# Kernel tuning notes

Hardware: AMD Instinct MI355X
Metric: run time of the kernel (lower is better)

The kernel has to match this reference:

```python
import jax, jax.numpy as jnp
import numpy as np
import math

N_EMBD = 1024
N_HEAD = 16
B, T, T_PLAN = 2, 2048, 512
EPS = 1e-5


def _layernorm(x, g, b):
    m = jnp.mean(x, axis=-1, keepdims=True)
    v = jnp.mean(jnp.square(x - m), axis=-1, keepdims=True)
    return (x - m) * jax.lax.rsqrt(v + EPS) * g + b


def setup_inputs() -> dict:
    key = jax.random.key(0)
    ks = jax.random.split(key, 16)
    C = N_EMBD
    s = 0.02
    inp = {
        "x": jax.random.normal(ks[0], (B, T, C), jnp.float32),
        "plan_hidden": jax.random.normal(ks[1], (B, T_PLAN, C), jnp.float32),
        "ln1_g": jnp.ones((C,), jnp.float32), "ln1_b": jnp.zeros((C,), jnp.float32),
        # weights stored as [in, out] (torch Linear applies x @ W.T)
        "c_attn_w": s * jax.random.normal(ks[2], (C, 3 * C), jnp.float32),
        "c_attn_b": jnp.zeros((3 * C,), jnp.float32),
        "attn_proj_w": s * jax.random.normal(ks[3], (C, C), jnp.float32),
        "attn_proj_b": jnp.zeros((C,), jnp.float32),
        "ln2_g": jnp.ones((C,), jnp.float32), "ln2_b": jnp.zeros((C,), jnp.float32),
        "q_w": s * jax.random.normal(ks[4], (C, C), jnp.float32), "q_b": jnp.zeros((C,), jnp.float32),
        "k_w": s * jax.random.normal(ks[5], (C, C), jnp.float32), "k_b": jnp.zeros((C,), jnp.float32),
        "v_w": s * jax.random.normal(ks[6], (C, C), jnp.float32), "v_b": jnp.zeros((C,), jnp.float32),
        "ca_proj_w": s * jax.random.normal(ks[7], (C, C), jnp.float32),
        "ca_proj_b": jnp.zeros((C,), jnp.float32),
        "ln3_g": jnp.ones((C,), jnp.float32), "ln3_b": jnp.zeros((C,), jnp.float32),
        "fc_w": s * jax.random.normal(ks[8], (C, 4 * C), jnp.float32),
        "fc_b": jnp.zeros((4 * C,), jnp.float32),
        "mlp_proj_w": s * jax.random.normal(ks[9], (4 * C, C), jnp.float32),
        "mlp_proj_b": jnp.zeros((C,), jnp.float32),
    }
    return inp


def _split_heads(t, n_head):  # [B,T,C] -> [B,H,T,D]
    Bs, Ts, Cs = t.shape
    return t.reshape(Bs, Ts, n_head, Cs // n_head).transpose(0, 2, 1, 3)


def _merge_heads(t):  # [B,H,T,D] -> [B,T,C]
    Bs, H, Ts, D = t.shape
    return t.transpose(0, 2, 1, 3).reshape(Bs, Ts, H * D)


def _self_attn(x, c_attn_w, c_attn_b, proj_w, proj_b):
    Bs, Ts, C = x.shape
    qkv = x @ c_attn_w + c_attn_b
    q, k, v = jnp.split(qkv, 3, axis=-1)
    q, k, v = (_split_heads(t, N_HEAD) for t in (q, k, v))
    scale = 1.0 / math.sqrt(C // N_HEAD)
    att = jnp.einsum("bhqd,bhkd->bhqk", q, k) * scale
    mask = jnp.tril(jnp.ones((Ts, Ts), bool))
    att = jnp.where(mask, att, -jnp.inf)
    att = jax.nn.softmax(att, axis=-1)
    y = jnp.einsum("bhqk,bhkd->bhqd", att, v)
    return _merge_heads(y) @ proj_w + proj_b


def _cross_attn(x, plan, q_w, q_b, k_w, k_b, v_w, v_b, proj_w, proj_b):
    C = x.shape[-1]
    q = _split_heads(x @ q_w + q_b, N_HEAD)
    k = _split_heads(plan @ k_w + k_b, N_HEAD)
    v = _split_heads(plan @ v_w + v_b, N_HEAD)
    scale = 1.0 / math.sqrt(C // N_HEAD)
    att = jax.nn.softmax(jnp.einsum("bhqd,bhkd->bhqk", q, k) * scale, axis=-1)
    y = jnp.einsum("bhqk,bhkd->bhqd", att, v)
    return _merge_heads(y) @ proj_w + proj_b


def reference(x, plan_hidden, ln1_g, ln1_b, c_attn_w, c_attn_b, attn_proj_w, attn_proj_b,
              ln2_g, ln2_b, q_w, q_b, k_w, k_b, v_w, v_b, ca_proj_w, ca_proj_b,
              ln3_g, ln3_b, fc_w, fc_b, mlp_proj_w, mlp_proj_b):
    x = x + _self_attn(_layernorm(x, ln1_g, ln1_b), c_attn_w, c_attn_b, attn_proj_w, attn_proj_b)
    x = x + _cross_attn(_layernorm(x, ln2_g, ln2_b), plan_hidden,
                        q_w, q_b, k_w, k_b, v_w, v_b, ca_proj_w, ca_proj_b)
    h = _layernorm(x, ln3_g, ln3_b)
    h = jax.nn.gelu(h @ fc_w + fc_b, approximate=False) @ mlp_proj_w + mlp_proj_b
    return x + h
```

## Files before the change

kernel.cpp:

```cpp
#include <hip/hip_runtime.h>
#include <stdint.h>

typedef __bf16 bf16;
typedef __bf16 bf16x4 __attribute__((ext_vector_type(4)));
typedef __bf16 bf16x8 __attribute__((ext_vector_type(8)));
typedef float  f32x4  __attribute__((ext_vector_type(4)));

#define DEVI __device__ __forceinline__

DEVI void gll16(const void* g, void* l) {
  __builtin_amdgcn_global_load_lds(
      (const __attribute__((address_space(1))) void*)g,
      (__attribute__((address_space(3))) void*)l,
      16, 0, 0);
}

DEVI f32x4 mfma16(bf16x8 a, bf16x8 b, f32x4 c) {
  return __builtin_amdgcn_mfma_f32_16x16x32_bf16(a, b, c, 0, 0, 0);
}

__global__ void k_conv_bf16(const float* __restrict__ in, bf16* __restrict__ out, int n4) {
  int i = blockIdx.x * 256 + threadIdx.x;
  if (i < n4) {
    f32x4 v = ((const f32x4*)in)[i];
    bf16x4 o;
    o[0] = (bf16)v[0]; o[1] = (bf16)v[1]; o[2] = (bf16)v[2]; o[3] = (bf16)v[3];
    ((bf16x4*)out)[i] = o;
  }
}

__global__ void k_concat2(const float* __restrict__ a, const float* __restrict__ b,
                          float* __restrict__ out, int n) {
  int i = blockIdx.x * 256 + threadIdx.x;
  if (i < n) out[i] = a[i];
  else if (i < 2 * n) out[i] = b[i - n];
}

DEVI void wt_body(char* arena, const float* __restrict__ W, bf16* __restrict__ WT,
                  int K, int N, int bx, int by, int tid) {
  float (*t)[65] = reinterpret_cast<float(*)[65]>(arena);
  int bn = bx * 64, bk = by * 64;
  int tx = tid & 63, ty = tid >> 6;
#pragma unroll
  for (int i = 0; i < 16; ++i)
    t[ty + i * 4][tx] = W[(size_t)(bk + ty + i * 4) * N + bn + tx];
  __syncthreads();
#pragma unroll
  for (int i = 0; i < 16; ++i)
    WT[(size_t)(bn + ty + i * 4) * K + bk + tx] = (bf16)t[tx][ty + i * 4];
}

DEVI void ln_body(char* arena, const float* __restrict__ x, const float* __restrict__ g,
                  const float* __restrict__ b, bf16* __restrict__ out, int row, int tid) {
  float* ps  = (float*)arena;
  float* psq = ps + 4;
  f32x4 v = ((const f32x4*)(x + (size_t)row * 1024))[tid];
  float s = v[0] + v[1] + v[2] + v[3];
  float sq = v[0]*v[0] + v[1]*v[1] + v[2]*v[2] + v[3]*v[3];
#pragma unroll
  for (int m = 1; m < 64; m <<= 1) {
    s  += __shfl_xor(s, m, 64);
    sq += __shfl_xor(sq, m, 64);
  }
  int w = tid >> 6;
  if ((tid & 63) == 0) { ps[w] = s; psq[w] = sq; }
  __syncthreads();
  s  = ps[0] + ps[1] + ps[2] + ps[3];
  sq = psq[0] + psq[1] + psq[2] + psq[3];
  float mean = s * (1.f / 1024.f);
  float rs = rsqrtf(sq * (1.f / 1024.f) - mean * mean + 1e-5f);
  f32x4 gv = ((const f32x4*)g)[tid];
  f32x4 bv = ((const f32x4*)b)[tid];
  bf16x4 o;
#pragma unroll
  for (int i = 0; i < 4; ++i) o[i] = (bf16)((v[i] - mean) * rs * gv[i] + bv[i]);
  ((bf16x4*)(out + (size_t)row * 1024))[tid] = o;
}

__global__ __launch_bounds__(256)
void k_ln(const float* __restrict__ x, const float* __restrict__ g,
          const float* __restrict__ b, bf16* __restrict__ out) {
  __shared__ __align__(16) char arena[64];
  ln_body(arena, x, g, b, out, blockIdx.x, threadIdx.x);
}

__global__ __launch_bounds__(256)
void mega_ln_wt(const float* __restrict__ x, const float* __restrict__ g,
                const float* __restrict__ b, bf16* __restrict__ out,
                const float* __restrict__ W, bf16* __restrict__ WT,
                int K, int N, int wgx) {
  __shared__ __align__(16) char arena[16640];
  if ((int)blockIdx.x < 4096) {
    ln_body(arena, x, g, b, out, blockIdx.x, threadIdx.x);
  } else {
    int wid = blockIdx.x - 4096;
    wt_body(arena, W, WT, K, N, wid % wgx, wid / wgx, threadIdx.x);
  }
}

template <int EPI>
DEVI void gemm_s_body(char* arena, const bf16* __restrict__ A, const bf16* __restrict__ BT,
                      const float* __restrict__ bias, void* __restrict__ Cout,
                      int M, int N, int K, const float* __restrict__ Xres,
                      int nwg, int bid) {
  char (*SA)[8192]  = reinterpret_cast<char(*)[8192]>(arena);
  char (*SB)[16384] = reinterpret_cast<char(*)[16384]>(arena + 16384);
  const int tid = threadIdx.x;
  const int lane = tid & 63;
  const int w = tid >> 6;
  const int wr = w >> 1, wc = w & 1;
  const int lr = lane & 15, lg = lane >> 4;
  const int nk = K >> 6;

  const int q = nwg >> 3, r = nwg & 7;
  const int xcd = bid & 7, loc = bid >> 3;
  const int wg = (xcd < r ? xcd * (q + 1) : r * (q + 1) + (xcd - r) * q) + loc;
  const int gy = M >> 6;
  const int m0 = (wg % gy) << 6, n0 = (wg / gy) << 7;

  const int c8 = tid & 7;
  const int hrb = tid >> 3;
  auto stgA = [&](int buf, int ktc) {
#pragma unroll
    for (int i = 0; i < 2; ++i) {
      int hr = i * 32 + hrb;
      const bf16* s = A + (size_t)(m0 + hr) * K + ((size_t)ktc << 6) + ((c8 ^ (hr & 7)) << 3);
      gll16(s, &SA[buf][(i * 256 + tid) * 16]);
    }
  };
  auto stgB = [&](int buf, int ktc) {
#pragma unroll
    for (int i = 0; i < 4; ++i) {
      int hr = i * 32 + hrb;
      const bf16* s = BT + (size_t)(n0 + hr) * K + ((size_t)ktc << 6) + ((c8 ^ (hr & 7)) << 3);
      gll16(s, &SB[buf][(i * 256 + tid) * 16]);
    }
  };
  auto rdf = [&](const char* base, int rloc, int ks) -> bf16x8 {
    return *(const bf16x8*)(base + rloc * 128 + (((ks << 6) + (lg << 4)) ^ ((rloc & 7) << 4)));
  };

  f32x4 acc[2][4] = {};

  stgA(0, 0); stgB(0, 0);
  __syncthreads();
  for (int kt = 0; kt < nk; ++kt) {
    const int cur = kt & 1;
    if (kt + 1 < nk) { stgA(cur ^ 1, kt + 1); stgB(cur ^ 1, kt + 1); }
    bf16x8 af[2][2], bfr[4][2];
#pragma unroll
    for (int i = 0; i < 2; ++i)
#pragma unroll
      for (int ks = 0; ks < 2; ++ks)
        af[i][ks] = rdf(SA[cur], wr * 32 + i * 16 + lr, ks);
#pragma unroll
    for (int j = 0; j < 4; ++j)
#pragma unroll
      for (int ks = 0; ks < 2; ++ks)
        bfr[j][ks] = rdf(SB[cur], wc * 64 + j * 16 + lr, ks);
#pragma unroll
    for (int i = 0; i < 2; ++i)
#pragma unroll
      for (int j = 0; j < 4; ++j)
#pragma unroll
        for (int ks = 0; ks < 2; ++ks)
          acc[i][j] = mfma16(af[i][ks], bfr[j][ks], acc[i][j]);
    __syncthreads();
  }

  float* of = (float*)Cout;
  bf16*  ob = (bf16*)Cout;
#pragma unroll
  for (int j = 0; j < 4; ++j) {
    int gn = n0 + wc * 64 + j * 16 + lr;
    float bv = bias[gn];
#pragma unroll
    for (int i = 0; i < 2; ++i) {
      int gmb = m0 + wr * 32 + i * 16 + lg * 4;
#pragma unroll
      for (int rr = 0; rr < 4; ++rr) {
        size_t idx = (size_t)(gmb + rr) * N + gn;
        float v = acc[i][j][rr] + bv;
        if (EPI == 0) ob[idx] = (bf16)v;
        else if (EPI == 1) of[idx] += v;
        else if (EPI == 3) of[idx] = Xres[idx] + v;
        else {
          float ge = 0.5f * v * (1.f + erff(v * 0.70710678f));
          ob[idx] = (bf16)ge;
        }
      }
    }
  }
}

template <int EPI>
__global__ __launch_bounds__(256, 3)
void k_gemm_s(const bf16* __restrict__ A, const bf16* __restrict__ BT,
              const float* __restrict__ bias, void* __restrict__ Cout,
              int M, int N, int K, const float* __restrict__ Xres) {
  __shared__ __align__(16) char arena[49152];
  gemm_s_body<EPI>(arena, A, BT, bias, Cout, M, N, K, Xres, gridDim.x, blockIdx.x);
}

__global__ __launch_bounds__(256, 3)
void mega_gemmA2(const bf16* __restrict__ A, const bf16* __restrict__ BT,
                 const float* __restrict__ bias, void* __restrict__ Cout,
                 const float* __restrict__ Xres,
                 const float* __restrict__ qw, bf16* __restrict__ qwt,
                 const float* __restrict__ kw, bf16* __restrict__ kwt,
                 const float* __restrict__ vw, bf16* __restrict__ vwt) {
  __shared__ __align__(16) char arena[49152];
  if ((int)blockIdx.x < 512) {
    gemm_s_body<3>(arena, A, BT, bias, Cout, 4096, 1024, 1024, Xres, 512, blockIdx.x);
  } else {
    int wid = blockIdx.x - 512;
    const float* W = wid < 256 ? qw : (wid < 512 ? kw : vw);
    bf16* WT = wid < 256 ? qwt : (wid < 512 ? kwt : vwt);
    int sub = wid & 255;
    wt_body(arena, W, WT, 1024, 1024, sub & 15, sub >> 4, threadIdx.x);
  }
}

__global__ __launch_bounds__(256, 3)
void mega_gemmB2(const bf16* __restrict__ A, const bf16* __restrict__ BT,
                 const float* __restrict__ bias, void* __restrict__ Cout,
                 const float* __restrict__ mw, bf16* __restrict__ mwt) {
  __shared__ __align__(16) char arena[49152];
  if ((int)blockIdx.x < 512) {
    gemm_s_body<1>(arena, A, BT, bias, Cout, 4096, 1024, 1024, nullptr, 512, blockIdx.x);
  } else {
    int wid = blockIdx.x - 512;
    wt_body(arena, mw, mwt, 4096, 1024, wid & 15, wid >> 4, threadIdx.x);
  }
}

template <int EPI>
__global__ __launch_bounds__(512, 2)
void k_gemm8(const bf16* __restrict__ A, const bf16* __restrict__ BT,
             const float* __restrict__ bias, void* __restrict__ Cout,
             int M, int N, int K) {
  __shared__ __align__(16) char SA[2][2][16384];
  __shared__ __align__(16) char SB[2][2][16384];
  const int tid = threadIdx.x;
  const int lane = tid & 63;
  const int w = tid >> 6;
  const int wm = w >> 2, wn = w & 3;
  const int lr = lane & 15, lg = lane >> 4;
  const int nk = K >> 6;

  const int nwg = gridDim.x;
  const int q = nwg >> 3, r = nwg & 7;
  const int xcd = blockIdx.x & 7, loc = blockIdx.x >> 3;
  const int wg = (xcd < r ? xcd * (q + 1) : r * (q + 1) + (xcd - r) * q) + loc;
  const int gy = M >> 8;
  const int m0 = (wg % gy) << 8, n0 = (wg / gy) << 8;

  const int c8 = tid & 7;
  auto stg = [&](char* dst, const bf16* src0, int base0, int half, int ktc) {
#pragma unroll
    for (int i = 0; i < 2; ++i) {
      int hr = i * 64 + (tid >> 3);
      const bf16* s = src0 + (size_t)(base0 + half * 128 + hr) * K + ((size_t)ktc << 6)
                    + ((c8 ^ (hr & 7)) << 3);
      gll16(s, dst + (i * 512 + tid) * 16);
    }
  };
  auto rdf = [&](const char* hbase, int rloc, int ks) -> bf16x8 {
    return *(const bf16x8*)(hbase + rloc * 128 + (((ks << 6) + (lg << 4)) ^ ((rloc & 7) << 4)));
  };

  f32x4 acc[8][4] = {};
  bf16x8 af[4][2], b0f[2][2], b1f[2][2];

  stg(SA[0][0], A, m0, 0, 0);
  stg(SB[0][0], BT, n0, 0, 0);
  stg(SB[0][1], BT, n0, 1, 0);
  stg(SA[0][1], A, m0, 1, 0);
  stg(SA[1][0], A, m0, 0, 1);
  stg(SB[1][0], BT, n0, 0, 1);
  asm volatile("s_waitcnt vmcnt(8)" ::: "memory");
  __builtin_amdgcn_s_barrier();

  for (int kt = 0; kt < nk; ++kt) {
    const int cur = kt & 1;
    const char* hA0 = SA[cur][0]; const char* hA1 = SA[cur][1];
    const char* hB0 = SB[cur][0]; const char* hB1 = SB[cur][1];
    const int tn  = (kt + 1 < nk) ? kt + 1 : nk - 1;
    const int tn2 = (kt + 2 < nk) ? kt + 2 : nk - 1;

    stg(SB[(kt + 1) & 1][1], BT, n0, 1, tn);
    asm volatile("s_waitcnt vmcnt(8)" ::: "memory");
#pragma unroll
    for (int i = 0; i < 4; ++i) {
      int rl = i * 32 + wm * 16 + lr;
#pragma unroll
      for (int ks = 0; ks < 2; ++ks) af[i][ks] = rdf(hA0, rl, ks);
    }
#pragma unroll
    for (int j = 0; j < 2; ++j) {
      int rl = j * 64 + wn * 16 + lr;
#pragma unroll
      for (int ks = 0; ks < 2; ++ks) b0f[j][ks] = rdf(hB0, rl, ks);
    }
    __builtin_amdgcn_s_barrier();
    __builtin_amdgcn_s_setprio(1);
#pragma unroll
    for (int i = 0; i < 4; ++i)
#pragma unroll
      for (int j = 0; j < 2; ++j)
#pragma unroll
        for (int ks = 0; ks < 2; ++ks)
          acc[i][j] = mfma16(af[i][ks], b0f[j][ks], acc[i][j]);
    __builtin_amdgcn_s_setprio(0);

    stg(SA[(kt + 1) & 1][1], A, m0, 1, tn);
    asm volatile("s_waitcnt vmcnt(8)" ::: "memory");
#pragma unroll
    for (int j = 0; j < 2; ++j) {
      int rl = j * 64 + wn * 16 + lr;
#pragma unroll
      for (int ks = 0; ks < 2; ++ks) b1f[j][ks] = rdf(hB1, rl, ks);
    }
    __builtin_amdgcn_s_barrier();
    __builtin_amdgcn_s_setprio(1);
#pragma unroll
    for (int i = 0; i < 4; ++i)
#pragma unroll
      for (int j = 0; j < 2; ++j)
#pragma unroll
        for (int ks = 0; ks < 2; ++ks)
          acc[i][2 + j] = mfma16(af[i][ks], b1f[j][ks], acc[i][2 + j]);
    __builtin_amdgcn_s_setprio(0);

    stg(SA[cur][0], A, m0, 0, tn2);
#pragma unroll
    for (int i = 0; i < 4; ++i) {
      int rl = i * 32 + wm * 16 + lr;
#pragma unroll
      for (int ks = 0; ks < 2; ++ks) af[i][ks] = rdf(hA1, rl, ks);
    }
    __builtin_amdgcn_s_barrier();
    __builtin_amdgcn_s_setprio(1);
#pragma unroll
    for (int i = 0; i < 4; ++i)
#pragma unroll
      for (int j = 0; j < 2; ++j)
#pragma unroll
        for (int ks = 0; ks < 2; ++ks)
          acc[4 + i][j] = mfma16(af[i][ks], b0f[j][ks], acc[4 + i][j]);
    __builtin_amdgcn_s_setprio(0);

    stg(SB[cur][0], BT, n0, 0, tn2);
    asm volatile("s_waitcnt vmcnt(8)" ::: "memory");
    __builtin_amdgcn_s_barrier();
    __builtin_amdgcn_s_setprio(1);
#pragma unroll
    for (int i = 0; i < 4; ++i)
#pragma unroll
      for (int j = 0; j < 2; ++j)
#pragma unroll
        for (int ks = 0; ks < 2; ++ks)
          acc[4 + i][2 + j] = mfma16(af[i][ks], b1f[j][ks], acc[4 + i][2 + j]);
    __builtin_amdgcn_s_setprio(0);
  }

  float* of = (float*)Cout;
  bf16*  ob = (bf16*)Cout;
#pragma unroll
  for (int ni = 0; ni < 4; ++ni) {
    int gn = n0 + (ni >> 1) * 128 + (ni & 1) * 64 + wn * 16 + lr;
    float bv = bias[gn];
#pragma unroll
    for (int mi = 0; mi < 8; ++mi) {
      int gmb = m0 + (mi >> 2) * 128 + (mi & 3) * 32 + wm * 16 + lg * 4;
#pragma unroll
      for (int rr = 0; rr < 4; ++rr) {
        size_t idx = (size_t)(gmb + rr) * N + gn;
        float v = acc[mi][ni][rr] + bv;
        if (EPI == 0) ob[idx] = (bf16)v;
        else if (EPI == 1) of[idx] += v;
        else {
          float ge = 0.5f * v * (1.f + erff(v * 0.70710678f));
          ob[idx] = (bf16)ge;
        }
      }
    }
  }
}

template <bool CAUSAL>
DEVI void attn_body(char* arena, int id,
                    const bf16* __restrict__ Qb, int ldq, int qcol0,
                    const bf16* __restrict__ Kb, int kcol0,
                    const bf16* __restrict__ Vb, int vcol0,
                    int ldkv, int qlen, int kvlen,
                    bf16* __restrict__ Ob, int ldo, float scale) {
  char (*Klds)[8192]   = reinterpret_cast<char(*)[8192]>(arena);
  bf16 (*VT)[64][68]   = reinterpret_cast<bf16(*)[64][68]>(arena + 16384);
  const int tid = threadIdx.x;
  const int lane = tid & 63;
  const int w = tid >> 6;
  const int lr = lane & 15, lg = lane >> 4;

  int h, b, qt;
  if (CAUSAL) {
    int low = id & 255;
    h = low & 15; b = (low >> 4) & 1;
    int q3 = low >> 5;
    qt = (id >> 8) ? (8 + q3) : (7 - q3);
  } else {
    h = id & 15; b = (id >> 4) & 1; qt = id >> 5;
  }

  const int qbase = qt * 128;
  const int kvbase = b * kvlen;
  const int nkv = CAUSAL ? (2 * qt + 2) : (kvlen >> 6);
  const int mask_from = CAUSAL ? (nkv - 2) : 0x7fffffff;

  bf16x8 qf[2][2];
#pragma unroll
  for (int g = 0; g < 2; ++g)
#pragma unroll
    for (int kk = 0; kk < 2; ++kk)
      qf[g][kk] = *(const bf16x8*)(Qb + (size_t)(b * qlen + qbase + w * 32 + g * 16 + lr) * ldq
                                   + qcol0 + h * 64 + kk * 32 + lg * 8);

  f32x4 o[2][4] = {};
  float mrun[2] = {-3.0e38f, -3.0e38f};
  float lsum[2] = {0.f, 0.f};

  bf16x8 vr0, vr1;
  const int vkv = lane;
  const int vd0 = (tid >> 6) * 16;
  const bf16* Vbase = Vb + vcol0 + h * 64 + vd0;

  auto stageK = [&](int buf, int kvt) {
#pragma unroll
    for (int t = 0; t < 2; ++t) {
      int r = t * 32 + (tid >> 3);
      int pb = (tid & 7) * 16;
      const char* gs = (const char*)(Kb + (size_t)(kvbase + kvt * 64 + r) * ldkv + kcol0 + h * 64)
                       + (pb ^ ((r & 7) << 4));
      gll16(gs, &Klds[buf][t * 4096 + tid * 16]);
    }
  };
  auto loadV = [&](int kvt) {
    const bf16* vp = Vbase + (size_t)(kvbase + kvt * 64 + vkv) * ldkv;
    vr0 = *(const bf16x8*)vp;
    vr1 = *(const bf16x8*)(vp + 8);
  };
  auto writeV = [&](int buf) {
#pragma unroll
    for (int i = 0; i < 8; ++i) VT[buf][vd0 + i][vkv] = vr0[i];
#pragma unroll
    for (int i = 0; i < 8; ++i) VT[buf][vd0 + 8 + i][vkv] = vr1[i];
  };

  stageK(0, 0);
  loadV(0);
  writeV(0);
  __syncthreads();

  int cur = 0;
  for (int kvt = 0; kvt < nkv; ++kvt) {
    if (kvt + 1 < nkv) { stageK(cur ^ 1, kvt + 1); loadV(kvt + 1); }

    f32x4 s[2][4] = {};
#pragma unroll
    for (int sub = 0; sub < 4; ++sub) {
      int row = sub * 16 + lr;
#pragma unroll
      for (int kk = 0; kk < 2; ++kk) {
        bf16x8 kf = *(const bf16x8*)&Klds[cur][(row << 7) + ((kk * 64 + lg * 16) ^ ((row & 7) << 4))];
        s[0][sub] = mfma16(kf, qf[0][kk], s[0][sub]);
        s[1][sub] = mfma16(kf, qf[1][kk], s[1][sub]);
      }
    }

    const bool domask = CAUSAL && (kvt >= mask_from);
    bf16x8 pa[2][2];
#pragma unroll
    for (int g = 0; g < 2; ++g) {
      const int qg = qbase + w * 32 + g * 16 + lr;
      float pmax = -3.0e38f;
#pragma unroll
      for (int sub = 0; sub < 4; ++sub)
#pragma unroll
        for (int j = 0; j < 4; ++j) {
          float v = s[g][sub][j] * scale;
          if (domask) {
            int kvg = kvt * 64 + sub * 16 + lg * 4 + j;
            if (kvg > qg) v = -3.0e38f;
          }
          s[g][sub][j] = v;
          pmax = fmaxf(pmax, v);
        }
      pmax = fmaxf(pmax, __shfl_xor(pmax, 16, 64));
      pmax = fmaxf(pmax, __shfl_xor(pmax, 32, 64));
      float mnew = mrun[g];
      if (__any(pmax - mrun[g] > 8.f)) {
        mnew = fmaxf(mrun[g], pmax);
        float alpha = __expf(mrun[g] - mnew);
        lsum[g] *= alpha;
        float al[4];
#pragma unroll
        for (int j = 0; j < 4; ++j) {
          int src = (lane & 48) | (lg * 4 + j);
          al[j] = __int_as_float(__builtin_amdgcn_ds_bpermute(src << 2, __float_as_int(alpha)));
        }
#pragma unroll
        for (int dt = 0; dt < 4; ++dt)
#pragma unroll
          for (int j = 0; j < 4; ++j) o[g][dt][j] *= al[j];
      }
      float psum = 0.f;
#pragma unroll
      for (int sub = 0; sub < 4; ++sub)
#pragma unroll
        for (int j = 0; j < 4; ++j) {
          float p = __expf(s[g][sub][j] - mnew);
          s[g][sub][j] = p;
          psum += p;
        }
      psum += __shfl_xor(psum, 16, 64);
      psum += __shfl_xor(psum, 32, 64);
      lsum[g] += psum;
      mrun[g] = mnew;
#pragma unroll
      for (int sp = 0; sp < 2; ++sp) {
#pragma unroll
        for (int j = 0; j < 4; ++j) {
          pa[g][sp][j]     = (bf16)s[g][2 * sp][j];
          pa[g][sp][4 + j] = (bf16)s[g][2 * sp + 1][j];
        }
      }
    }

#pragma unroll
    for (int sp = 0; sp < 2; ++sp) {
#pragma unroll
      for (int dt = 0; dt < 4; ++dt) {
        int d = dt * 16 + lr;
        bf16x4 va  = *(const bf16x4*)&VT[cur][d][sp * 32 + lg * 4];
        bf16x4 vb2 = *(const bf16x4*)&VT[cur][d][sp * 32 + 16 + lg * 4];
        bf16x8 vf = __builtin_shufflevector(va, vb2, 0, 1, 2, 3, 4, 5, 6, 7);
        o[0][dt] = mfma16(pa[0][sp], vf, o[0][dt]);
        o[1][dt] = mfma16(pa[1][sp], vf, o[1][dt]);
      }
    }

    if (kvt + 1 < nkv) writeV(cur ^ 1);
    __syncthreads();
    cur ^= 1;
  }

#pragma unroll
  for (int g = 0; g < 2; ++g) {
    float il[4];
#pragma unroll
    for (int j = 0; j < 4; ++j) {
      int src = (lane & 48) | (lg * 4 + j);
      float ls = __int_as_float(__builtin_amdgcn_ds_bpermute(src << 2, __float_as_int(lsum[g])));
      il[j] = 1.0f / ls;
    }
#pragma unroll
    for (int dt = 0; dt < 4; ++dt)
#pragma unroll
      for (int j = 0; j < 4; ++j) {
        int gq = b * qlen + qbase + w * 32 + g * 16 + lg * 4 + j;
        Ob[(size_t)gq * ldo + h * 64 + dt * 16 + lr] = (bf16)(o[g][dt][j] * il[j]);
      }
  }
}

template <bool CAUSAL>
__global__ __launch_bounds__(256)
void mega_attn_wt(const bf16* __restrict__ Qb, int ldq, int qcol0,
                  const bf16* __restrict__ Kb, int kcol0,
                  const bf16* __restrict__ Vb, int vcol0,
                  int ldkv, int qlen, int kvlen,
                  bf16* __restrict__ Ob, int ldo, float scale,
                  const float* __restrict__ W, bf16* __restrict__ WT) {
  __shared__ __align__(16) char arena[33792];
  if ((int)blockIdx.x < 512) {
    attn_body<CAUSAL>(arena, blockIdx.x, Qb, ldq, qcol0, Kb, kcol0, Vb, vcol0,
                      ldkv, qlen, kvlen, Ob, ldo, scale);
  } else {
    int wid = blockIdx.x - 512;
    wt_body(arena, W, WT, 1024, 1024, wid & 15, wid >> 4, threadIdx.x);
  }
}

extern "C" void kernel_launch(void* const* d_in, const int* in_sizes, int n_in,
                              void* d_out, int out_size, void* d_ws, size_t ws_size,
                              hipStream_t stream) {
  (void)in_sizes; (void)n_in; (void)out_size; (void)ws_size;
  const float* x        = (const float*)d_in[0];
  const float* plan     = (const float*)d_in[1];
  const float* ln1_g    = (const float*)d_in[2];
  const float* ln1_b    = (const float*)d_in[3];
  const float* c_attn_w = (const float*)d_in[4];
  const float* c_attn_b = (const float*)d_in[5];
  const float* aproj_w  = (const float*)d_in[6];
  const float* aproj_b  = (const float*)d_in[7];
  const float* ln2_g    = (const float*)d_in[8];
  const float* ln2_b    = (const float*)d_in[9];
  const float* q_w      = (const float*)d_in[10];
  const float* q_b      = (const float*)d_in[11];
  const float* k_w      = (const float*)d_in[12];
  const float* k_b      = (const float*)d_in[13];
  const float* v_w      = (const float*)d_in[14];
  const float* v_b      = (const float*)d_in[15];
  const float* ca_w     = (const float*)d_in[16];
  const float* ca_b     = (const float*)d_in[17];
  const float* ln3_g    = (const float*)d_in[18];
  const float* ln3_b    = (const float*)d_in[19];
  const float* fc_w     = (const float*)d_in[20];
  const float* fc_b     = (const float*)d_in[21];
  const float* mp_w     = (const float*)d_in[22];
  const float* mp_b     = (const float*)d_in[23];

  char* ws = (char*)d_ws;
  bf16*  wbuf   = (bf16*)(ws);
  bf16*  lnb    = (bf16*)(ws + (8ull << 20));
  bf16*  planb  = (bf16*)(ws + (16ull << 20));
  bf16*  yb     = (bf16*)(ws + (18ull << 20));
  char*  rega   = ws + (26ull << 20);
  float* biaskv = (float*)(ws + (58ull << 20));
  bf16* qkv  = (bf16*)rega;
  bf16* qwt  = (bf16*)rega;
  bf16* kwt  = (bf16*)(rega + (2ull << 20));
  bf16* vwt  = (bf16*)(rega + (4ull << 20));
  bf16* kvc  = (bf16*)(rega + (8ull << 20));
  bf16* co   = (bf16*)(rega + (12ull << 20));
  bf16* hmid = (bf16*)rega;
  float* xw = (float*)d_out;

  k_conv_bf16<<<1024, 256, 0, stream>>>(plan, planb, 262144);
  k_concat2<<<8, 256, 0, stream>>>(k_b, v_b, biaskv, 1024);

  mega_ln_wt<<<4096 + 768, 256, 0, stream>>>(x, ln1_g, ln1_b, lnb,
                                             c_attn_w, wbuf, 1024, 3072, 48);
  k_gemm8<0><<<192, 512, 0, stream>>>(lnb, wbuf, c_attn_b, qkv, 4096, 3072, 1024);
  mega_attn_wt<true><<<512 + 256, 256, 0, stream>>>(qkv, 3072, 0, qkv, 1024, qkv, 2048,
                                                    3072, 2048, 2048, yb, 1024, 0.125f,
                                                    aproj_w, wbuf);
  mega_gemmA2<<<512 + 768, 256, 0, stream>>>(yb, wbuf, aproj_b, xw, x,
                                             q_w, qwt, k_w, kwt, v_w, vwt);

  k_ln<<<4096, 256, 0, stream>>>(xw, ln2_g, ln2_b, lnb);
  k_gemm_s<0><<<512, 256, 0, stream>>>(lnb, qwt, q_b, yb, 4096, 1024, 1024, nullptr);
  k_gemm_s<0><<<256, 256, 0, stream>>>(planb, kwt, biaskv, kvc, 1024, 2048, 1024, nullptr);
  mega_attn_wt<false><<<512 + 256, 256, 0, stream>>>(yb, 1024, 0, kvc, 0, kvc, 1024,
                                                     2048, 2048, 512, co, 1024, 0.125f,
                                                     ca_w, wbuf);
  mega_gemmB2<<<512 + 1024, 256, 0, stream>>>(co, wbuf, ca_b, xw, mp_w, yb);

  mega_ln_wt<<<4096 + 1024, 256, 0, stream>>>(xw, ln3_g, ln3_b, lnb,
                                              fc_w, wbuf, 1024, 4096, 64);
  k_gemm8<2><<<256, 512, 0, stream>>>(lnb, wbuf, fc_b, hmid, 4096, 4096, 1024);
  k_gemm_s<1><<<512, 256, 0, stream>>>(hmid, yb, mp_b, xw, 4096, 1024, 4096, nullptr);
}
```

Baseline: 315.6 us.

## Fold small prep kernels and independent GEMMs into shared launches

Merges the plan fp32-to-bf16 conversion and the k/v bias concatenation into the first LayerNorm/transpose launch. Runs the cross-attention Q GEMM and the KV GEMM together in one kernel. Moves the fc weight transpose into the causal attention launch so ln3 becomes a plain LayerNorm. Transposed weights are reassigned to buffers that are free at each stage. This removes several kernel launches and overlaps weight prep with compute. The cost is tighter buffer aliasing and more complex lifetime dependencies across stages.

```diff
diff --git a/kernel.cpp b/kernel.cpp
--- a/kernel.cpp
+++ b/kernel.cpp
@@ -17,23 +17,6 @@
 
 DEVI f32x4 mfma16(bf16x8 a, bf16x8 b, f32x4 c) {
   return __builtin_amdgcn_mfma_f32_16x16x32_bf16(a, b, c, 0, 0, 0);
-}
-
-__global__ void k_conv_bf16(const float* __restrict__ in, bf16* __restrict__ out, int n4) {
-  int i = blockIdx.x * 256 + threadIdx.x;
-  if (i < n4) {
-    f32x4 v = ((const f32x4*)in)[i];
-    bf16x4 o;
-    o[0] = (bf16)v[0]; o[1] = (bf16)v[1]; o[2] = (bf16)v[2]; o[3] = (bf16)v[3];
-    ((bf16x4*)out)[i] = o;
-  }
-}
-
-__global__ void k_concat2(const float* __restrict__ a, const float* __restrict__ b,
-                          float* __restrict__ out, int n) {
-  int i = blockIdx.x * 256 + threadIdx.x;
-  if (i < n) out[i] = a[i];
-  else if (i < 2 * n) out[i] = b[i - n];
 }
 
 DEVI void wt_body(char* arena, const float* __restrict__ W, bf16* __restrict__ WT,
@@ -85,16 +68,28 @@
 }
 
 __global__ __launch_bounds__(256)
-void mega_ln_wt(const float* __restrict__ x, const float* __restrict__ g,
-                const float* __restrict__ b, bf16* __restrict__ out,
-                const float* __restrict__ W, bf16* __restrict__ WT,
-                int K, int N, int wgx) {
+void mega_misc(const float* __restrict__ x, const float* __restrict__ g,
+               const float* __restrict__ b, bf16* __restrict__ out,
+               const float* __restrict__ W, bf16* __restrict__ WT,
+               const float* __restrict__ plan, bf16* __restrict__ planb,
+               const float* __restrict__ kb, const float* __restrict__ vb,
+               float* __restrict__ biaskv) {
   __shared__ __align__(16) char arena[16640];
-  if ((int)blockIdx.x < 4096) {
-    ln_body(arena, x, g, b, out, blockIdx.x, threadIdx.x);
+  const int bid = blockIdx.x, tid = threadIdx.x;
+  if (bid < 4096) {
+    ln_body(arena, x, g, b, out, bid, tid);
+  } else if (bid < 4864) {
+    int wid = bid - 4096;
+    wt_body(arena, W, WT, 1024, 3072, wid % 48, wid / 48, tid);
+  } else if (bid < 5888) {
+    int i = (bid - 4864) * 256 + tid;
+    f32x4 v = ((const f32x4*)plan)[i];
+    bf16x4 o;
+    o[0] = (bf16)v[0]; o[1] = (bf16)v[1]; o[2] = (bf16)v[2]; o[3] = (bf16)v[3];
+    ((bf16x4*)planb)[i] = o;
   } else {
-    int wid = blockIdx.x - 4096;
-    wt_body(arena, W, WT, K, N, wid % wgx, wid / wgx, threadIdx.x);
+    int i = (bid - 5888) * 256 + tid;
+    biaskv[i] = i < 1024 ? kb[i] : vb[i - 1024];
   }
 }
 
@@ -231,6 +226,19 @@
   } else {
     int wid = blockIdx.x - 512;
     wt_body(arena, mw, mwt, 4096, 1024, wid & 15, wid >> 4, threadIdx.x);
+  }
+}
+
+__global__ __launch_bounds__(256, 3)
+void mega_gemmC2(const bf16* __restrict__ Aq, const bf16* __restrict__ qwt,
+                 const float* __restrict__ qb, void* __restrict__ qxo,
+                 const bf16* __restrict__ Ap, const bf16* __restrict__ kwt,
+                 const float* __restrict__ bkv, void* __restrict__ kvo) {
+  __shared__ __align__(16) char arena[49152];
+  if ((int)blockIdx.x < 512) {
+    gemm_s_body<0>(arena, Aq, qwt, qb, qxo, 4096, 1024, 1024, nullptr, 512, blockIdx.x);
+  } else {
+    gemm_s_body<0>(arena, Ap, kwt, bkv, kvo, 1024, 2048, 1024, nullptr, 256, blockIdx.x - 512);
   }
 }
 
@@ -573,21 +581,25 @@
   }
 }
 
-template <bool CAUSAL>
+template <bool CAUSAL, bool WT2>
 __global__ __launch_bounds__(256)
 void mega_attn_wt(const bf16* __restrict__ Qb, int ldq, int qcol0,
                   const bf16* __restrict__ Kb, int kcol0,
                   const bf16* __restrict__ Vb, int vcol0,
                   int ldkv, int qlen, int kvlen,
                   bf16* __restrict__ Ob, int ldo, float scale,
-                  const float* __restrict__ W, bf16* __restrict__ WT) {
+                  const float* __restrict__ W1, bf16* __restrict__ WT1,
+                  const float* __restrict__ W2, bf16* __restrict__ WT2b) {
   __shared__ __align__(16) char arena[33792];
   if ((int)blockIdx.x < 512) {
     attn_body<CAUSAL>(arena, blockIdx.x, Qb, ldq, qcol0, Kb, kcol0, Vb, vcol0,
                       ldkv, qlen, kvlen, Ob, ldo, scale);
-  } else {
+  } else if ((int)blockIdx.x < 768) {
     int wid = blockIdx.x - 512;
-    wt_body(arena, W, WT, 1024, 1024, wid & 15, wid >> 4, threadIdx.x);
+    wt_body(arena, W1, WT1, 1024, 1024, wid & 15, wid >> 4, threadIdx.x);
+  } else if (WT2) {
+    int wid = blockIdx.x - 768;
+    wt_body(arena, W2, WT2b, 1024, 4096, wid & 63, wid >> 6, threadIdx.x);
   }
 }
 
@@ -630,34 +642,30 @@
   bf16* qkv  = (bf16*)rega;
   bf16* qwt  = (bf16*)rega;
   bf16* kwt  = (bf16*)(rega + (2ull << 20));
-  bf16* vwt  = (bf16*)(rega + (4ull << 20));
   bf16* kvc  = (bf16*)(rega + (8ull << 20));
   bf16* co   = (bf16*)(rega + (12ull << 20));
   bf16* hmid = (bf16*)rega;
+  bf16* aprojT = lnb;
+  bf16* caT    = lnb;
+  bf16* fcT    = wbuf;
+  bf16* mpT    = yb;
   float* xw = (float*)d_out;
 
-  k_conv_bf16<<<1024, 256, 0, stream>>>(plan, planb, 262144);
-  k_concat2<<<8, 256, 0, stream>>>(k_b, v_b, biaskv, 1024);
-
-  mega_ln_wt<<<4096 + 768, 256, 0, stream>>>(x, ln1_g, ln1_b, lnb,
-                                             c_attn_w, wbuf, 1024, 3072, 48);
+  mega_misc<<<5896, 256, 0, stream>>>(x, ln1_g, ln1_b, lnb, c_attn_w, wbuf,
+                                      plan, planb, k_b, v_b, biaskv);
   k_gemm8<0><<<192, 512, 0, stream>>>(lnb, wbuf, c_attn_b, qkv, 4096, 3072, 1024);
-  mega_attn_wt<true><<<512 + 256, 256, 0, stream>>>(qkv, 3072, 0, qkv, 1024, qkv, 2048,
-                                                    3072, 2048, 2048, yb, 1024, 0.125f,
-                                                    aproj_w, wbuf);
-  mega_gemmA2<<<512 + 768, 256, 0, stream>>>(yb, wbuf, aproj_b, xw, x,
-                                             q_w, qwt, k_w, kwt, v_w, vwt);
-
+  mega_attn_wt<true, true><<<512 + 256 + 1024, 256, 0, stream>>>(
+      qkv, 3072, 0, qkv, 1024, qkv, 2048, 3072, 2048, 2048, yb, 1024, 0.125f,
+      aproj_w, aprojT, fc_w, fcT);
+  mega_gemmA2<<<512 + 768, 256, 0, stream>>>(yb, aprojT, aproj_b, xw, x,
+                                             q_w, qwt, k_w, kwt, v_w, kwt + (1u << 20));
   k_ln<<<4096, 256, 0, stream>>>(xw, ln2_g, ln2_b, lnb);
-  k_gemm_s<0><<<512, 256, 0, stream>>>(lnb, qwt, q_b, yb, 4096, 1024, 1024, nullptr);
-  k_gemm_s<0><<<256, 256, 0, stream>>>(planb, kwt, biaskv, kvc, 1024, 2048, 1024, nullptr);
-  mega_attn_wt<false><<<512 + 256, 256, 0, stream>>>(yb, 1024, 0, kvc, 0, kvc, 1024,
-                                                     2048, 2048, 512, co, 1024, 0.125f,
-                                                     ca_w, wbuf);
-  mega_gemmB2<<<512 + 1024, 256, 0, stream>>>(co, wbuf, ca_b, xw, mp_w, yb);
-
-  mega_ln_wt<<<4096 + 1024, 256, 0, stream>>>(xw, ln3_g, ln3_b, lnb,
-                                              fc_w, wbuf, 1024, 4096, 64);
-  k_gemm8<2><<<256, 512, 0, stream>>>(lnb, wbuf, fc_b, hmid, 4096, 4096, 1024);
-  k_gemm_s<1><<<512, 256, 0, stream>>>(hmid, yb, mp_b, xw, 4096, 1024, 4096, nullptr);
-}
+  mega_gemmC2<<<768, 256, 0, stream>>>(lnb, qwt, q_b, yb, planb, kwt, biaskv, kvc);
+  mega_attn_wt<false, false><<<512 + 256, 256, 0, stream>>>(
+      yb, 1024, 0, kvc, 0, kvc, 1024, 2048, 2048, 512, co, 1024, 0.125f,
+      ca_w, caT, nullptr, nullptr);
+  mega_gemmB2<<<512 + 1024, 256, 0, stream>>>(co, caT, ca_b, xw, mp_w, mpT);
+  k_ln<<<4096, 256, 0, stream>>>(xw, ln3_g, ln3_b, lnb);
+  k_gemm8<2><<<256, 512, 0, stream>>>(lnb, fcT, fc_b, hmid, 4096, 4096, 1024);
+  k_gemm_s<1><<<512, 256, 0, stream>>>(hmid, mpT, mp_b, xw, 4096, 1024, 4096, nullptr);
+}
```

Result: faster. 295.8 us (median of 2 runs) (-6.3%).
